# Kernel optimization log

Hardware: AMD Instinct MI355X
Metric: run time of the kernel (lower is better)

## Reference

```python
import jax, jax.numpy as jnp
import numpy as np

N_BITS = 8
Q_LEVELS = N_BITS ** 2 - 1  # note: original uses n_bits**2 - 1, not 2**n_bits - 1
GRID_RES = (128, 512, 2048)  # 2**7, 2**9, 2**11
BITWIDTH = 6
CODE_SIZE = 4


def _qround(x, axis):
    mn = jnp.min(x, axis=axis, keepdims=True)
    mx = jnp.max(x, axis=axis, keepdims=True)
    scale = jnp.maximum(mx - mn, 1e-8) / Q_LEVELS
    return jnp.round((x - mn) / scale) * scale + mn


def _ste(q, x):
    # straight-through estimator: forward q, gradient of x
    return jax.lax.stop_gradient(q - x) + x


def _qalinear(x, w, b):
    w_q = _ste(_qround(w, (-2, -1)), w)
    b_q = _ste(_qround(b, -1), b)
    return x @ w_q + b_q


def _grid(coords, indices, codebook, res):
    # coords: [N] in [-1, 1]; indices: [res, 2**bitwidth]; codebook: [2**bitwidth, code_size]
    soft_grid = jax.nn.softmax(indices, axis=-1) @ codebook           # [res, C]
    max_grid = codebook[jnp.argmax(indices, axis=1)]                  # [res, C]
    grid = _ste(max_grid, soft_grid)
    c = (coords + 1.0) / 2.0 * (res - 1)
    left = jnp.minimum(jnp.floor(c), res - 2).astype(jnp.int32)
    right = jnp.maximum(jnp.ceil(c), 1).astype(jnp.int32)
    w = (c - left)[..., None]                                         # [N, 1]
    return (1.0 - w) * grid[left] + w * grid[right]                   # [N, C]


def setup_inputs() -> dict:
    key = jax.random.key(0)
    ks = jax.random.split(key, 20)
    N = 1 << 20
    x_coord = jax.random.uniform(ks[0], (N, 1), jnp.float32, -1.0, 1.0)
    x_feat = jax.random.uniform(ks[1], (N, 1), jnp.float32, -1.0, 1.0)
    x = jnp.concatenate([x_feat, x_coord], axis=-1)  # last dim is the grid coordinate
    inp = {"x": x}
    for gi, res in enumerate(GRID_RES):
        inp[f"cb{gi}"] = 0.01 * jax.random.normal(ks[2 + 2 * gi], (2 ** BITWIDTH, CODE_SIZE), jnp.float32)
        inp[f"ind{gi}"] = 0.01 * jax.random.normal(ks[3 + 2 * gi], (res, 2 ** BITWIDTH), jnp.float32)
    dims = [(5, 64), (64, 64), (64, 64), (64, 64), (64, 1)]
    for li, (di, do) in enumerate(dims):
        inp[f"w{li}"] = (2 * jax.random.uniform(ks[8 + 2 * li], (di, do), jnp.float32) - 1) / np.sqrt(di)
        inp[f"b{li}"] = (2 * jax.random.uniform(ks[9 + 2 * li], (do,), jnp.float32) - 1) / np.sqrt(di)
    return inp


def reference(x, cb0, ind0, cb1, ind1, cb2, ind2,
              w0, b0, w1, b1, w2, b2, w3, b3, w4, b4):
    coords = x[..., -1]
    g = (_grid(coords, ind0, cb0, GRID_RES[0])
         + _grid(coords, ind1, cb1, GRID_RES[1])
         + _grid(coords, ind2, cb2, GRID_RES[2]))           # [N, 4]
    h = jnp.concatenate([g, x[..., :-1]], axis=-1)          # [N, 5]
    h = _qalinear(h, w0, b0)
    for w, b in ((w1, b1), (w2, b2), (w3, b3)):
        h = _qalinear(jax.nn.gelu(h, approximate=False), w, b)
    h = _qalinear(jax.nn.gelu(h, approximate=False), w4, b4)
    return jnp.tanh(h)
```

## Files before the change

### kernel.cpp

```cpp
#include <hip/hip_runtime.h>
#include <hip/hip_bf16.h>
#include <math.h>

#define WQ0 0
#define BQ0 320
#define WQ1 384
#define BQ1 4480
#define WQ2 4544
#define BQ2 8640
#define WQ3 8704
#define BQ3 12800
#define WQ4 12864
#define BQ4 12928
#define GT0 12932
#define GT1 13444
#define GT2 15492
#define FRAG_OFF 23684
#define NFRAG 28
#define WSCALE 64.0f
#define WINV   0.015625f

typedef _Float16 f16x8 __attribute__((ext_vector_type(8)));
typedef float floatx4 __attribute__((ext_vector_type(4)));
typedef float floatx2 __attribute__((ext_vector_type(2)));
typedef unsigned int uintx4 __attribute__((ext_vector_type(4)));

__device__ inline floatx4 mfma16(f16x8 a, f16x8 b, floatx4 c) {
    return __builtin_amdgcn_mfma_f32_16x16x32_f16(a, b, c, 0, 0, 0);
}
__device__ inline floatx2 splat2(float c) { return (floatx2){c, c}; }

__device__ inline floatx2 gelu2(floatx2 x) {
    floatx2 ax = __builtin_elementwise_abs(x);
    floatx2 z  = ax * splat2(0.70710678118654752f);
    floatx2 den = __builtin_elementwise_fma(z, splat2(0.47047f), splat2(1.0f));
    floatx2 t;
    t.x = __builtin_amdgcn_rcpf(den.x);
    t.y = __builtin_amdgcn_rcpf(den.y);
    floatx2 p = __builtin_elementwise_fma(t, splat2(0.7478556f), splat2(-0.0958798f));
    p = __builtin_elementwise_fma(t, p, splat2(0.3480242f));
    p = p * t;
    floatx2 ea = (z * z) * splat2(-1.44269504088896f);
    floatx2 e;
    e.x = __builtin_amdgcn_exp2f(ea.x);
    e.y = __builtin_amdgcn_exp2f(ea.y);
    floatx2 er = __builtin_elementwise_fma(-p, e, splat2(1.0f));
    return __builtin_elementwise_fma(ax, er, x) * splat2(0.5f);
}

__device__ inline float tanh_fast(float x) {
    float e = __builtin_amdgcn_exp2f(x * 2.88539008177793f);
    return fmaf(-2.0f, __builtin_amdgcn_rcpf(e + 1.0f), 1.0f);
}

__device__ void block_minmax(float mn, float mx, float* omn, float* omx,
                             float* smn, float* smx) {
    __syncthreads();
    #pragma unroll
    for (int off = 32; off > 0; off >>= 1) {
        mn = fminf(mn, __shfl_down(mn, off));
        mx = fmaxf(mx, __shfl_down(mx, off));
    }
    int wid = threadIdx.x >> 6, lane = threadIdx.x & 63;
    if (lane == 0) { smn[wid] = mn; smx[wid] = mx; }
    __syncthreads();
    if (threadIdx.x == 0) {
        float a = smn[0], b = smx[0];
        for (int i = 1; i < 4; ++i) { a = fminf(a, smn[i]); b = fmaxf(b, smx[i]); }
        smn[0] = a; smx[0] = b;
    }
    __syncthreads();
    *omn = smn[0]; *omx = smx[0];
}

__device__ void quantize_tensor(const float* __restrict__ src, int n,
                                float* __restrict__ dst, float* smn, float* smx) {
    float mn = 3.4e38f, mx = -3.4e38f;
    for (int i = threadIdx.x; i < n; i += blockDim.x) {
        float v = src[i];
        mn = fminf(mn, v); mx = fmaxf(mx, v);
    }
    float gmn, gmx;
    block_minmax(mn, mx, &gmn, &gmx, smn, smx);
    float scale = fmaxf(gmx - gmn, 1e-8f) / 63.0f;
    for (int i = threadIdx.x; i < n; i += blockDim.x) {
        float v = src[i];
        dst[i] = rintf((v - gmn) / scale) * scale + gmn;
    }
}

__global__ void vinr_prep(
    const float* __restrict__ cb0, const float* __restrict__ ind0,
    const float* __restrict__ cb1, const float* __restrict__ ind1,
    const float* __restrict__ cb2, const float* __restrict__ ind2,
    const float* __restrict__ w0, const float* __restrict__ b0,
    const float* __restrict__ w1, const float* __restrict__ b1,
    const float* __restrict__ w2, const float* __restrict__ b2,
    const float* __restrict__ w3, const float* __restrict__ b3,
    const float* __restrict__ w4, const float* __restrict__ b4,
    float* __restrict__ ws)
{
    __shared__ float smn[4], smx[4];
    if (blockIdx.x < 10) {
        switch (blockIdx.x) {
            case 0: quantize_tensor(w0, 320, ws + WQ0, smn, smx); break;
            case 1: quantize_tensor(b0, 64, ws + BQ0, smn, smx); break;
            case 2: quantize_tensor(w1, 4096, ws + WQ1, smn, smx); break;
            case 3: quantize_tensor(b1, 64, ws + BQ1, smn, smx); break;
            case 4: quantize_tensor(w2, 4096, ws + WQ2, smn, smx); break;
            case 5: quantize_tensor(b2, 64, ws + BQ2, smn, smx); break;
            case 6: quantize_tensor(w3, 4096, ws + WQ3, smn, smx); break;
            case 7: quantize_tensor(b3, 64, ws + BQ3, smn, smx); break;
            case 8: quantize_tensor(w4, 64, ws + WQ4, smn, smx); break;
            case 9: quantize_tensor(b4, 1, ws + BQ4, smn, smx); break;
        }
    } else if (blockIdx.x < 21) {
        int r = (int)(blockIdx.x - 10) * 256 + (int)threadIdx.x;
        const float* ind = nullptr; const float* cb = nullptr; float* dst = nullptr;
        if (r < 128)       { ind = ind0 + r * 64;          cb = cb0; dst = ws + GT0 + r * 4; }
        else if (r < 640)  { int rr = r - 128;  ind = ind1 + rr * 64; cb = cb1; dst = ws + GT1 + rr * 4; }
        else if (r < 2688) { int rr = r - 640;  ind = ind2 + rr * 64; cb = cb2; dst = ws + GT2 + rr * 4; }
        if (dst) {
            float best = -3.4e38f; int bi = 0;
            for (int j = 0; j < 64; ++j) {
                float v = ind[j];
                if (v > best) { best = v; bi = j; }
            }
            #pragma unroll
            for (int d = 0; d < 4; ++d) dst[d] = cb[bi * 4 + d];
        }
    } else if (blockIdx.x < 45) {
        if (threadIdx.x < 64) {
            int fi = (int)blockIdx.x - 21;
            int lane = (int)threadIdx.x;
            int l = fi >> 3, s = (fi >> 2) & 1, ft = fi & 3;
            const float* w = (l == 0) ? w1 : (l == 1) ? w2 : w3;
            float mn = 3.4e38f, mx = -3.4e38f;
            for (int i = lane; i < 4096; i += 64) {
                float v = w[i];
                mn = fminf(mn, v); mx = fmaxf(mx, v);
            }
            #pragma unroll
            for (int off = 32; off > 0; off >>= 1) {
                mn = fminf(mn, __shfl_xor(mn, off));
                mx = fmaxf(mx, __shfl_xor(mx, off));
            }
            float scale = fmaxf(mx - mn, 1e-8f) / 63.0f;
            int q = lane >> 4, m15 = lane & 15;
            int n = ft * 16 + m15;
            f16x8 hi, lo;
            #pragma unroll
            for (int j = 0; j < 8; ++j) {
                int k = s * 32 + q * 8 + j;
                float v = w[k * 64 + n];
                v = (rintf((v - mn) / scale) * scale + mn) * WSCALE;
                _Float16 hb = (_Float16)v;
                hi[j] = hb;
                lo[j] = (_Float16)(v - (float)hb);
            }
            f16x8* base = (f16x8*)(ws + FRAG_OFF);
            base[fi * 64 + lane] = hi;
            base[NFRAG * 64 + fi * 64 + lane] = lo;
        }
    } else {
        int wv = (int)threadIdx.x >> 6;
        int lane = (int)threadIdx.x & 63;
        if (wv < 4) {
            float mn = 3.4e38f, mx = -3.4e38f;
            for (int i = lane; i < 320; i += 64) {
                float v = w0[i];
                mn = fminf(mn, v); mx = fmaxf(mx, v);
            }
            #pragma unroll
            for (int off = 32; off > 0; off >>= 1) {
                mn = fminf(mn, __shfl_xor(mn, off));
                mx = fmaxf(mx, __shfl_xor(mx, off));
            }
            float scale = fmaxf(mx - mn, 1e-8f) / 63.0f;
            int q = lane >> 4, m15 = lane & 15;
            int n = wv * 16 + m15;
            f16x8 hi, lo;
            #pragma unroll
            for (int j = 0; j < 8; ++j) {
                int k = q * 8 + j;
                float v = 0.0f;
                if (k < 5) {
                    float vv = w0[k * 64 + n];
                    v = (rintf((vv - mn) / scale) * scale + mn) * WSCALE;
                }
                _Float16 hb = (_Float16)v;
                hi[j] = hb;
                lo[j] = (_Float16)(v - (float)hb);
            }
            f16x8* base = (f16x8*)(ws + FRAG_OFF);
            base[(24 + wv) * 64 + lane] = hi;
            base[NFRAG * 64 + (24 + wv) * 64 + lane] = lo;
        }
    }
}

#define LSTR 68

__device__ inline f16x8 cvt8(float4 xa, float4 xb) {
    f16x8 r;
    r[0] = (_Float16)xa.x; r[1] = (_Float16)xa.y;
    r[2] = (_Float16)xa.z; r[3] = (_Float16)xa.w;
    r[4] = (_Float16)xb.x; r[5] = (_Float16)xb.y;
    r[6] = (_Float16)xb.z; r[7] = (_Float16)xb.w;
    return r;
}

__global__ __launch_bounds__(256, 4) void vinr_main(
    const float* __restrict__ x, const float* __restrict__ ws,
    float* __restrict__ out, int N)
{
    __shared__ __align__(16) float hlds[4 * 32 * LSTR];
    int wave = threadIdx.x >> 6, lane = threadIdx.x & 63;
    int q = lane >> 4, m15 = lane & 15;
    int p = lane & 31, half = lane >> 5, j0 = half << 5;
    float* slice = hlds + wave * (32 * LSTR);

    int idx = (int)blockIdx.x * 128 + wave * 32 + p;
    int idxc = min(idx, N - 1);
    float2 xr = ((const float2*)x)[idxc];
    float feat  = xr.x;
    float coord = xr.y;

    float g0 = 0.f, g1 = 0.f, g2 = 0.f, g3 = 0.f;
    const int RES[3]  = {128, 512, 2048};
    const int GOFF[3] = {GT0, GT1, GT2};
    #pragma unroll
    for (int gi = 0; gi < 3; ++gi) {
        int res = RES[gi];
        float c = (coord + 1.0f) * 0.5f * (float)(res - 1);
        int left  = min((int)floorf(c), res - 2);
        int right = max((int)ceilf(c), 1);
        float w = c - (float)left;
        const float4* gt = (const float4*)(ws + GOFF[gi]);
        float4 gl = gt[left];
        float4 gr = gt[right];
        float wm = 1.0f - w;
        g0 += wm * gl.x + w * gr.x;
        g1 += wm * gl.y + w * gr.y;
        g2 += wm * gl.z + w * gr.z;
        g3 += wm * gl.w + w * gr.w;
    }

    const f16x8* fh = (const f16x8*)(ws + FRAG_OFF);
    const f16x8* fl = fh + NFRAG * 64;
    f16x8 zfrag = __builtin_bit_cast(f16x8, (uintx4){0u, 0u, 0u, 0u});

    if (half == 0) {
        float* row = slice + p * LSTR;
        *(float4*)row = make_float4(g0, g1, g2, g3);
        *(float4*)(row + 4) = make_float4(feat, 0.0f, 0.0f, 0.0f);
    }

    {
        f16x8 Wh[4], Wl[4];
        #pragma unroll
        for (int ft = 0; ft < 4; ++ft) {
            Wh[ft] = fh[(24 + ft) * 64 + lane];
            Wl[ft] = fl[(24 + ft) * 64 + lane];
        }
        f16x8 B[2];
        #pragma unroll
        for (int pt = 0; pt < 2; ++pt) {
            B[pt] = zfrag;
            if (q == 0) {
                const float* ap = slice + (pt * 16 + m15) * LSTR;
                B[pt] = cvt8(*(const float4*)ap, *(const float4*)(ap + 4));
            }
        }
        floatx4 acc[4][2];
        #pragma unroll
        for (int ft = 0; ft < 4; ++ft)
            #pragma unroll
            for (int pt = 0; pt < 2; ++pt)
                acc[ft][pt] = (floatx4){0.f, 0.f, 0.f, 0.f};
        #pragma unroll
        for (int ft = 0; ft < 4; ++ft)
            #pragma unroll
            for (int pt = 0; pt < 2; ++pt) {
                acc[ft][pt] = mfma16(Wh[ft], B[pt], acc[ft][pt]);
                acc[ft][pt] = mfma16(Wl[ft], B[pt], acc[ft][pt]);
            }
        #pragma unroll
        for (int ft = 0; ft < 4; ++ft) {
            float4 b4 = *(const float4*)(ws + BQ0 + ft * 16 + q * 4);
            #pragma unroll
            for (int pt = 0; pt < 2; ++pt) {
                floatx4 av = acc[ft][pt];
                floatx2 a01 = __builtin_elementwise_fma((floatx2){av[0], av[1]},
                                  splat2(WINV), (floatx2){b4.x, b4.y});
                floatx2 a23 = __builtin_elementwise_fma((floatx2){av[2], av[3]},
                                  splat2(WINV), (floatx2){b4.z, b4.w});
                floatx2 v01 = gelu2(a01);
                floatx2 v23 = gelu2(a23);
                *(float4*)(slice + (pt * 16 + m15) * LSTR + ft * 16 + q * 4) =
                    make_float4(v01.x, v01.y, v23.x, v23.y);
            }
        }
    }

    const int BQL[3] = {BQ1, BQ2, BQ3};
    #pragma unroll 1
    for (int l = 0; l < 3; ++l) {
        floatx4 acc[4][2];
        #pragma unroll
        for (int ft = 0; ft < 4; ++ft)
            #pragma unroll
            for (int pt = 0; pt < 2; ++pt)
                acc[ft][pt] = (floatx4){0.f, 0.f, 0.f, 0.f};

        #pragma unroll
        for (int s = 0; s < 2; ++s) {
            f16x8 Wh[4], Wl[4];
            #pragma unroll
            for (int ft = 0; ft < 4; ++ft) {
                int fi = (l * 2 + s) * 4 + ft;
                Wh[ft] = fh[fi * 64 + lane];
                Wl[ft] = fl[fi * 64 + lane];
            }
            f16x8 B[2];
            #pragma unroll
            for (int pt = 0; pt < 2; ++pt) {
                const float* ap = slice + (pt * 16 + m15) * LSTR + s * 32 + q * 8;
                B[pt] = cvt8(*(const float4*)ap, *(const float4*)(ap + 4));
            }
            #pragma unroll
            for (int ft = 0; ft < 4; ++ft) {
                #pragma unroll
                for (int pt = 0; pt < 2; ++pt) {
                    acc[ft][pt] = mfma16(Wh[ft], B[pt], acc[ft][pt]);
                    acc[ft][pt] = mfma16(Wl[ft], B[pt], acc[ft][pt]);
                }
            }
        }
        #pragma unroll
        for (int ft = 0; ft < 4; ++ft) {
            float4 b4 = *(const float4*)(ws + BQL[l] + ft * 16 + q * 4);
            #pragma unroll
            for (int pt = 0; pt < 2; ++pt) {
                floatx4 av = acc[ft][pt];
                floatx2 a01 = __builtin_elementwise_fma((floatx2){av[0], av[1]},
                                  splat2(WINV), (floatx2){b4.x, b4.y});
                floatx2 a23 = __builtin_elementwise_fma((floatx2){av[2], av[3]},
                                  splat2(WINV), (floatx2){b4.z, b4.w});
                floatx2 v01 = gelu2(a01);
                floatx2 v23 = gelu2(a23);
                *(float4*)(slice + (pt * 16 + m15) * LSTR + ft * 16 + q * 4) =
                    make_float4(v01.x, v01.y, v23.x, v23.y);
            }
        }
    }

    {
        const floatx2* w4v = (const floatx2*)(ws + WQ4);
        float acc4 = (half == 0) ? ws[BQ4] : 0.0f;
        const float* row = slice + p * LSTR + j0;
        floatx2 a2 = splat2(0.0f);
        #pragma unroll
        for (int c = 0; c < 8; ++c) {
            float4 v = *(const float4*)(row + 4 * c);
            a2 = __builtin_elementwise_fma((floatx2){v.x, v.y}, w4v[(j0 >> 1) + 2 * c],     a2);
            a2 = __builtin_elementwise_fma((floatx2){v.z, v.w}, w4v[(j0 >> 1) + 2 * c + 1], a2);
        }
        acc4 += a2.x + a2.y;
        acc4 += __shfl_xor(acc4, 32);
        if (half == 0 && idx < N) out[idx] = tanh_fast(acc4);
    }
}

extern "C" void kernel_launch(void* const* d_in, const int* in_sizes, int n_in,
                              void* d_out, int out_size, void* d_ws, size_t ws_size,
                              hipStream_t stream) {
    const float* x    = (const float*)d_in[0];
    const float* cb0  = (const float*)d_in[1];
    const float* ind0 = (const float*)d_in[2];
    const float* cb1  = (const float*)d_in[3];
    const float* ind1 = (const float*)d_in[4];
    const float* cb2  = (const float*)d_in[5];
    const float* ind2 = (const float*)d_in[6];
    const float* w0 = (const float*)d_in[7],  * b0 = (const float*)d_in[8];
    const float* w1 = (const float*)d_in[9],  * b1 = (const float*)d_in[10];
    const float* w2 = (const float*)d_in[11], * b2 = (const float*)d_in[12];
    const float* w3 = (const float*)d_in[13], * b3 = (const float*)d_in[14];
    const float* w4 = (const float*)d_in[15], * b4 = (const float*)d_in[16];
    float* ws  = (float*)d_ws;
    float* out = (float*)d_out;

    int N = in_sizes[0] / 2;

    vinr_prep<<<46, 256, 0, stream>>>(cb0, ind0, cb1, ind1, cb2, ind2,
                                      w0, b0, w1, b1, w2, b2, w3, b3, w4, b4, ws);
    int blocks = (N + 127) / 128;
    vinr_main<<<blocks, 256, 0, stream>>>(x, ws, out, N);
}
```

Measured before the change: 245.8 us.

## Store inter-layer activations in LDS as packed fp16 and use fdot2 for final layer

Activations staged in shared memory between MLP layers are now written as packed fp16 pairs instead of fp32. This halves LDS footprint and traffic and removes the per-fragment float-to-half conversions before each MFMA. The final 64-to-1 layer uses a hi/lo fp16 split of the quantized w4, precomputed by an extra prep block, and evaluates with fdot2 instructions. Row stride changes to 38 words. Lower LDS use may also allow more resident waves. The final layer now reads fp16 activations instead of fp32, which adds a small precision loss.

```diff
diff --git a/kernel.cpp b/kernel.cpp
--- a/kernel.cpp
+++ b/kernel.cpp
@@ -17,10 +17,12 @@
 #define GT2 15492
 #define FRAG_OFF 23684
 #define NFRAG 28
+#define W4P 38020
 #define WSCALE 64.0f
 #define WINV   0.015625f
 
 typedef _Float16 f16x8 __attribute__((ext_vector_type(8)));
+typedef _Float16 f16x2 __attribute__((ext_vector_type(2)));
 typedef float floatx4 __attribute__((ext_vector_type(4)));
 typedef float floatx2 __attribute__((ext_vector_type(2)));
 typedef unsigned int uintx4 __attribute__((ext_vector_type(4)));
@@ -29,6 +31,27 @@
     return __builtin_amdgcn_mfma_f32_16x16x32_f16(a, b, c, 0, 0, 0);
 }
 __device__ inline floatx2 splat2(float c) { return (floatx2){c, c}; }
+
+__device__ inline unsigned int pack_f16(float a, float b) {
+    unsigned short ua = __builtin_bit_cast(unsigned short, (_Float16)a);
+    unsigned short ub = __builtin_bit_cast(unsigned short, (_Float16)b);
+    return (unsigned int)ua | ((unsigned int)ub << 16);
+}
+__device__ inline f16x8 frag_from(uint2 a, uint2 b) {
+    uintx4 u = {a.x, a.y, b.x, b.y};
+    return __builtin_bit_cast(f16x8, u);
+}
+__device__ inline f16x2 h2(unsigned int u) { return __builtin_bit_cast(f16x2, u); }
+
+#if __has_builtin(__builtin_amdgcn_fdot2)
+__device__ inline float fdot2f(f16x2 a, f16x2 b, float c) {
+    return __builtin_amdgcn_fdot2(a, b, c, false);
+}
+#else
+__device__ inline float fdot2f(f16x2 a, f16x2 b, float c) {
+    return fmaf((float)a[0], (float)b[0], fmaf((float)a[1], (float)b[1], c));
+}
+#endif
 
 __device__ inline floatx2 gelu2(floatx2 x) {
     floatx2 ax = __builtin_elementwise_abs(x);
@@ -162,7 +185,7 @@
             base[fi * 64 + lane] = hi;
             base[NFRAG * 64 + fi * 64 + lane] = lo;
         }
-    } else {
+    } else if (blockIdx.x == 45) {
         int wv = (int)threadIdx.x >> 6;
         int lane = (int)threadIdx.x & 63;
         if (wv < 4) {
@@ -196,29 +219,40 @@
             base[(24 + wv) * 64 + lane] = hi;
             base[NFRAG * 64 + (24 + wv) * 64 + lane] = lo;
         }
-    }
-}
-
-#define LSTR 68
-
-__device__ inline f16x8 cvt8(float4 xa, float4 xb) {
-    f16x8 r;
-    r[0] = (_Float16)xa.x; r[1] = (_Float16)xa.y;
-    r[2] = (_Float16)xa.z; r[3] = (_Float16)xa.w;
-    r[4] = (_Float16)xb.x; r[5] = (_Float16)xb.y;
-    r[6] = (_Float16)xb.z; r[7] = (_Float16)xb.w;
-    return r;
-}
+    } else {
+        if (threadIdx.x < 64) {
+            int lane = (int)threadIdx.x;
+            float v = w4[lane];
+            float mn = v, mx = v;
+            #pragma unroll
+            for (int off = 32; off > 0; off >>= 1) {
+                mn = fminf(mn, __shfl_xor(mn, off));
+                mx = fmaxf(mx, __shfl_xor(mx, off));
+            }
+            float scale = fmaxf(mx - mn, 1e-8f) / 63.0f;
+            if (lane < 32) {
+                float q0 = (rintf((w4[2 * lane] - mn) / scale) * scale + mn) * WSCALE;
+                float q1 = (rintf((w4[2 * lane + 1] - mn) / scale) * scale + mn) * WSCALE;
+                float h0 = (float)(_Float16)q0, h1 = (float)(_Float16)q1;
+                unsigned int* wsU = (unsigned int*)ws;
+                wsU[W4P + lane]      = pack_f16(q0, q1);
+                wsU[W4P + 32 + lane] = pack_f16(q0 - h0, q1 - h1);
+            }
+        }
+    }
+}
+
+#define PSTR 38
 
 __global__ __launch_bounds__(256, 4) void vinr_main(
     const float* __restrict__ x, const float* __restrict__ ws,
     float* __restrict__ out, int N)
 {
-    __shared__ __align__(16) float hlds[4 * 32 * LSTR];
+    __shared__ __align__(16) unsigned int hlds[4 * 32 * PSTR];
     int wave = threadIdx.x >> 6, lane = threadIdx.x & 63;
     int q = lane >> 4, m15 = lane & 15;
-    int p = lane & 31, half = lane >> 5, j0 = half << 5;
-    float* slice = hlds + wave * (32 * LSTR);
+    int p = lane & 31, half = lane >> 5;
+    unsigned int* slice = hlds + wave * (32 * PSTR);
 
     int idx = (int)blockIdx.x * 128 + wave * 32 + p;
     int idxc = min(idx, N - 1);
@@ -251,9 +285,9 @@
     f16x8 zfrag = __builtin_bit_cast(f16x8, (uintx4){0u, 0u, 0u, 0u});
 
     if (half == 0) {
-        float* row = slice + p * LSTR;
-        *(float4*)row = make_float4(g0, g1, g2, g3);
-        *(float4*)(row + 4) = make_float4(feat, 0.0f, 0.0f, 0.0f);
+        unsigned int* row = slice + p * PSTR;
+        *(uint2*)row       = make_uint2(pack_f16(g0, g1), pack_f16(g2, g3));
+        *(uint2*)(row + 2) = make_uint2(pack_f16(feat, 0.0f), 0u);
     }
 
     {
@@ -268,8 +302,8 @@
         for (int pt = 0; pt < 2; ++pt) {
             B[pt] = zfrag;
             if (q == 0) {
-                const float* ap = slice + (pt * 16 + m15) * LSTR;
-                B[pt] = cvt8(*(const float4*)ap, *(const float4*)(ap + 4));
+                const unsigned int* rp = slice + (pt * 16 + m15) * PSTR;
+                B[pt] = frag_from(*(const uint2*)rp, *(const uint2*)(rp + 2));
             }
         }
         floatx4 acc[4][2];
@@ -297,8 +331,8 @@
                                   splat2(WINV), (floatx2){b4.z, b4.w});
                 floatx2 v01 = gelu2(a01);
                 floatx2 v23 = gelu2(a23);
-                *(float4*)(slice + (pt * 16 + m15) * LSTR + ft * 16 + q * 4) =
-                    make_float4(v01.x, v01.y, v23.x, v23.y);
+                *(uint2*)(slice + (pt * 16 + m15) * PSTR + 8 * ft + 2 * q) =
+                    make_uint2(pack_f16(v01.x, v01.y), pack_f16(v23.x, v23.y));
             }
         }
     }
@@ -325,8 +359,9 @@
             f16x8 B[2];
             #pragma unroll
             for (int pt = 0; pt < 2; ++pt) {
-                const float* ap = slice + (pt * 16 + m15) * LSTR + s * 32 + q * 8;
-                B[pt] = cvt8(*(const float4*)ap, *(const float4*)(ap + 4));
+                const unsigned int* rp =
+                    slice + (pt * 16 + m15) * PSTR + 16 * s + 4 * q;
+                B[pt] = frag_from(*(const uint2*)rp, *(const uint2*)(rp + 2));
             }
             #pragma unroll
             for (int ft = 0; ft < 4; ++ft) {
@@ -349,24 +384,27 @@
                                   splat2(WINV), (floatx2){b4.z, b4.w});
                 floatx2 v01 = gelu2(a01);
                 floatx2 v23 = gelu2(a23);
-                *(float4*)(slice + (pt * 16 + m15) * LSTR + ft * 16 + q * 4) =
-                    make_float4(v01.x, v01.y, v23.x, v23.y);
+                *(uint2*)(slice + (pt * 16 + m15) * PSTR + 8 * ft + 2 * q) =
+                    make_uint2(pack_f16(v01.x, v01.y), pack_f16(v23.x, v23.y));
             }
         }
     }
 
     {
-        const floatx2* w4v = (const floatx2*)(ws + WQ4);
-        float acc4 = (half == 0) ? ws[BQ4] : 0.0f;
-        const float* row = slice + p * LSTR + j0;
-        floatx2 a2 = splat2(0.0f);
+        const unsigned int* wsU = (const unsigned int*)ws;
+        const unsigned int* base = slice + p * PSTR + 16 * half;
+        int wb = W4P + 16 * half;
+        float ah = 0.0f, al = 0.0f;
         #pragma unroll
         for (int c = 0; c < 8; ++c) {
-            float4 v = *(const float4*)(row + 4 * c);
-            a2 = __builtin_elementwise_fma((floatx2){v.x, v.y}, w4v[(j0 >> 1) + 2 * c],     a2);
-            a2 = __builtin_elementwise_fma((floatx2){v.z, v.w}, w4v[(j0 >> 1) + 2 * c + 1], a2);
-        }
-        acc4 += a2.x + a2.y;
+            uint2 r = *(const uint2*)(base + 2 * c);
+            f16x2 a0 = h2(r.x), a1 = h2(r.y);
+            ah = fdot2f(a0, h2(wsU[wb + 2 * c]),      ah);
+            ah = fdot2f(a1, h2(wsU[wb + 2 * c + 1]),  ah);
+            al = fdot2f(a0, h2(wsU[wb + 32 + 2 * c]),     al);
+            al = fdot2f(a1, h2(wsU[wb + 32 + 2 * c + 1]), al);
+        }
+        float acc4 = fmaf(ah + al, WINV, (half == 0) ? ws[BQ4] : 0.0f);
         acc4 += __shfl_xor(acc4, 32);
         if (half == 0 && idx < N) out[idx] = tanh_fast(acc4);
     }
@@ -392,7 +430,7 @@
 
     int N = in_sizes[0] / 2;
 
-    vinr_prep<<<46, 256, 0, stream>>>(cb0, ind0, cb1, ind1, cb2, ind2,
+    vinr_prep<<<47, 256, 0, stream>>>(cb0, ind0, cb1, ind1, cb2, ind2,
                                       w0, b0, w1, b1, w2, b2, w3, b3, w4, b4, ws);
     int blocks = (N + 127) / 128;
     vinr_main<<<blocks, 256, 0, stream>>>(x, ws, out, N);
```

Result: faster. 238.3 us (-3.0%).
